# Kernel optimization log

Hardware: AMD Instinct MI355X
Metric: run time of the kernel (lower is better)

Reference implementation:

```python
import jax, jax.numpy as jnp
import numpy as np

N_NODES = 80000
N_EDGES = 1280000
D_NODE = 128
D_EDGE = 32
HID = 64
OUT = 32
EPS_GEN = 1e-7
EPS_BN = 1e-5


def _lin_init(key, fan_in, fan_out):
    return (jax.random.normal(key, (fan_in, fan_out), jnp.float32) / np.sqrt(fan_in))


def setup_inputs() -> dict:
    key = jax.random.key(0)
    ks = jax.random.split(key, 20)
    inp = {
        "x": jax.random.normal(ks[0], (N_NODES, D_NODE), jnp.float32),
        "edge_index": jax.random.randint(ks[1], (2, N_EDGES), 0, N_NODES, jnp.int32),
        "edge_attr": jax.random.normal(ks[2], (N_EDGES, D_EDGE), jnp.float32),
        # encoders
        "node_W": _lin_init(ks[3], D_NODE, HID), "node_b": jnp.zeros((HID,), jnp.float32),
        "edge_W": _lin_init(ks[4], D_EDGE, HID), "edge_b": jnp.zeros((HID,), jnp.float32),
        # GENConv layer 1 MLP: [HID -> 2HID (bias=False)] -> BN -> ReLU -> [2HID -> HID (bias=False)]
        "c1_W1": _lin_init(ks[5], HID, 2 * HID), "c1_g": jnp.ones((2 * HID,), jnp.float32), "c1_be": jnp.zeros((2 * HID,), jnp.float32), "c1_W2": _lin_init(ks[6], 2 * HID, HID),
        # GENConv layer 2
        "c2_W1": _lin_init(ks[7], HID, 2 * HID), "c2_g": jnp.ones((2 * HID,), jnp.float32), "c2_be": jnp.zeros((2 * HID,), jnp.float32), "c2_W2": _lin_init(ks[8], 2 * HID, HID),
        # edge update linears on concat(3*HID)
        "l1_W": _lin_init(ks[9], 3 * HID, HID), "l1_b": jnp.zeros((HID,), jnp.float32),
        "l2_W": _lin_init(ks[10], 3 * HID, OUT), "l2_b": jnp.zeros((OUT,), jnp.float32),
    }
    return inp


def _scatter_softmax_agg(msg, dst, n_nodes):
    # SoftmaxAggregation with t=1: per-destination, per-feature softmax weights
    m = jax.ops.segment_max(msg, dst, num_segments=n_nodes)  # [N, H]
    m = jnp.where(jnp.isfinite(m), m, 0.0)                   # nodes w/o in-edges
    ex = jnp.exp(msg - m[dst])                               # [E, H]
    denom = jax.ops.segment_sum(ex, dst, num_segments=n_nodes)
    alpha = ex / (denom[dst] + 1e-16)
    return jax.ops.segment_sum(msg * alpha, dst, num_segments=n_nodes)


def _batchnorm(h, gamma, beta):
    mu = jnp.mean(h, axis=0)
    var = jnp.var(h, axis=0)
    return (h - mu) * jax.lax.rsqrt(var + EPS_BN) * gamma + beta


def _genconv(x, src, dst, edge_attr, W1, g, be, W2):
    msg = jax.nn.relu(x[src] + edge_attr) + EPS_GEN          # [E, HID]
    agg = _scatter_softmax_agg(msg, dst, x.shape[0])         # [N, HID]
    h = agg + x
    h = jax.nn.relu(_batchnorm(h @ W1, g, be))
    return h @ W2


def reference(x, edge_index, edge_attr, node_W, node_b, edge_W, edge_b,
              c1_W1, c1_g, c1_be, c1_W2, c2_W1, c2_g, c2_be, c2_W2,
              l1_W, l1_b, l2_W, l2_b):
    src, dst = edge_index[0], edge_index[1]
    ea = edge_attr @ edge_W + edge_b                          # [E, HID]
    h = x @ node_W + node_b                                   # [N, HID]

    convs = [(c1_W1, c1_g, c1_be, c1_W2), (c2_W1, c2_g, c2_be, c2_W2)]
    lins = [(l1_W, l1_b), (l2_W, l2_b)]
    for (W1, g, be, W2), (lW, lb) in zip(convs, lins):
        h = jax.nn.relu(_genconv(h, src, dst, ea, W1, g, be, W2))
        # dropout is identity in eval mode
        ef = jnp.concatenate([h[src], ea, h[dst]], axis=-1)   # [E, 3*HID]
        ea = ef @ lW + lb
    return h, ea
```

## Files before the change

### kernel.cpp

```cpp
#include <hip/hip_runtime.h>
#include <hip/hip_bf16.h>

#define N_NODES 80000
#define N_EDGES 1280000
constexpr int DN = 128;
constexpr int DE = 32;
constexpr int H  = 64;
constexpr int H2 = 128;
constexpr float EPS_GEN = 1e-7f;
constexpr float EPS_BN  = 1e-5f;

typedef _Float16 f16x8 __attribute__((ext_vector_type(8)));
typedef _Float16 f16x4 __attribute__((ext_vector_type(4)));
typedef float f32x4 __attribute__((ext_vector_type(4)));

__device__ __forceinline__ void atomAddF(float* p, float v) {
  __hip_atomic_fetch_add(p, v, __ATOMIC_RELAXED, __HIP_MEMORY_SCOPE_AGENT);
}

struct PrepDesc { const float* W; _Float16* img; int K; int OC; int blkStart; };
struct PrepAll { PrepDesc d[8]; };

__global__ void k_prep_all(PrepAll P) {
  int b = blockIdx.x;
  int i = 0;
#pragma unroll
  for (int t = 1; t < 8; ++t)
    if (P.d[t].blkStart <= b) i = t;
  const PrepDesc D = P.d[i];
  int idx = (b - D.blkStart) * 256 + threadIdx.x;
  if (idx >= D.K * D.OC) return;
  int nslabK = D.K >> 5;
  int j = idx & 7, m16 = (idx >> 3) & 15, kg = (idx >> 7) & 3;
  int slab = idx >> 9;
  int kk = slab % nslabK, n2 = slab / nslabK;
  int k = kk * 32 + kg * 8 + j, n = n2 * 16 + m16;
  D.img[idx] = (_Float16)D.W[k * D.OC + n];
}

template <int K, int OC, bool IN16, bool AFFINE, bool BIAS,
          bool RELU_OUT, bool OUT16, bool OUT32, bool SCATOUT, bool STATS>
__global__ __launch_bounds__(256) void k_dense(
    const void* __restrict__ Ain, const _Float16* __restrict__ wimg,
    const float* __restrict__ bias, const float* __restrict__ sums,
    const float* __restrict__ g, const float* __restrict__ be,
    const int* __restrict__ posmap,
    _Float16* __restrict__ out16, float* __restrict__ out32,
    float* __restrict__ sums_out) {
  constexpr int NK = K / 32, NF = OC / 16;
  __shared__ float sSC[AFFINE ? H2 : 1], sSH[AFFINE ? H2 : 1];
  __shared__ float sStat[STATS ? 1024 : 1];
  const int tid = threadIdx.x, wv = tid >> 6, lane = tid & 63;
  const int m16 = lane & 15, kg = lane >> 4;
  const int rowbase = blockIdx.x * 64 + wv * 16;
  if constexpr (AFFINE) {
    for (int i = tid; i < H2; i += 256) {
      float mu  = sums[i] * (1.0f / N_NODES);
      float var = sums[H2 + i] * (1.0f / N_NODES) - mu * mu;
      float sc  = rsqrtf(var + EPS_BN) * g[i];
      sSC[i] = sc;
      sSH[i] = be[i] - mu * sc;
    }
    __syncthreads();
  }
  const int arow = rowbase + m16;
  f32x4 acc[NF];
#pragma unroll
  for (int n2 = 0; n2 < NF; ++n2) {
    float bv = BIAS ? bias[n2 * 16 + m16] : 0.0f;
    acc[n2] = (f32x4){bv, bv, bv, bv};
  }
  const _Float16* wp = wimg + (size_t)lane * 8;
#pragma unroll
  for (int kk = 0; kk < NK; ++kk) {
    f16x8 a;
    if constexpr (IN16) {
      const _Float16* ap = (const _Float16*)Ain + (size_t)arow * K + kg * 8 + kk * 32;
      a = *(const f16x8*)ap;
      if constexpr (AFFINE) {
#pragma unroll
        for (int j = 0; j < 8; ++j) {
          int f = kg * 8 + kk * 32 + j;
          float v = fmaxf(fmaf((float)a[j], sSC[f], sSH[f]), 0.0f);
          a[j] = (_Float16)v;
        }
      }
    } else {
      const float* ap = (const float*)Ain + (size_t)arow * K + kg * 8 + kk * 32;
      float4 v0 = *(const float4*)ap;
      float4 v1 = *(const float4*)(ap + 4);
      a = (f16x8){(_Float16)v0.x, (_Float16)v0.y, (_Float16)v0.z, (_Float16)v0.w,
                  (_Float16)v1.x, (_Float16)v1.y, (_Float16)v1.z, (_Float16)v1.w};
    }
#pragma unroll
    for (int n2 = 0; n2 < NF; ++n2) {
      f16x8 bb = *(const f16x8*)(wp + ((size_t)(n2 * NK + kk) << 9));
      acc[n2] = __builtin_amdgcn_mfma_f32_16x16x32_f16(a, bb, acc[n2], 0, 0, 0);
    }
  }
#pragma unroll
  for (int n2 = 0; n2 < NF; ++n2)
#pragma unroll
    for (int r = 0; r < 4; ++r) {
      float o = acc[n2][r];
      if constexpr (RELU_OUT) o = fmaxf(o, 0.0f);
      int orow = rowbase + kg * 4 + r;
      if constexpr (SCATOUT) orow = posmap[orow];
      size_t oi = (size_t)orow * OC + n2 * 16 + m16;
      if constexpr (OUT16) out16[oi] = (_Float16)o;
      if constexpr (OUT32) out32[oi] = o;
    }
  if constexpr (STATS) {
    static_assert(!STATS || NF == 8, "STATS assumes OC==128");
#pragma unroll
    for (int n2 = 0; n2 < NF; ++n2) {
      float s = acc[n2][0] + acc[n2][1] + acc[n2][2] + acc[n2][3];
      float q = acc[n2][0] * acc[n2][0] + acc[n2][1] * acc[n2][1] +
                acc[n2][2] * acc[n2][2] + acc[n2][3] * acc[n2][3];
      s += __shfl_xor(s, 16); s += __shfl_xor(s, 32);
      q += __shfl_xor(q, 16); q += __shfl_xor(q, 32);
      if (kg == 0) {
        sStat[wv * 128 + n2 * 16 + m16] = s;
        sStat[512 + wv * 128 + n2 * 16 + m16] = q;
      }
    }
    __syncthreads();
    {
      int which = tid >> 7, f = tid & 127;
      const float* b0 = sStat + which * 512;
      float v = b0[f] + b0[128 + f] + b0[256 + f] + b0[384 + f];
      atomAddF(&sums_out[which * H2 + f], v);
    }
  }
}

template <int OC, typename OUT_T, int T, bool SCAT>
__global__ __launch_bounds__(256) void k_edge_upd_srt(
    const _Float16* __restrict__ h, const _Float16* __restrict__ ea,
    const int4* __restrict__ eidsQ,
    const _Float16* __restrict__ wimg, const float* __restrict__ lb,
    OUT_T* __restrict__ eout) {
  constexpr int NF = OC / 16;
  __shared__ _Float16 sWf[NF * 6 * 512];
  __shared__ int sS[T * 64], sD[T * 64];
  __shared__ int sE[SCAT ? T * 64 : 1];
  const int tid = threadIdx.x, wv = tid >> 6, lane = tid & 63;
  const int m16 = lane & 15, kg = lane >> 4;
  const int p0 = blockIdx.x * (T * 64);

  for (int i = tid; i < T * 64; i += 256) {
    int4 t = eidsQ[p0 + i];
    sS[i] = t.y;
    sD[i] = t.z;
    if constexpr (SCAT) sE[i] = t.x;
  }
  {
    const float4* s4 = (const float4*)wimg;
    float4* d4 = (float4*)sWf;
    constexpr int NV = NF * 6 * 512 / 8;
    for (int i = tid; i < NV; i += 256) d4[i] = s4[i];
  }
  __syncthreads();
  const _Float16* wp = sWf + (size_t)lane * 8;

  float bias_[NF];
#pragma unroll
  for (int n2 = 0; n2 < NF; ++n2) bias_[n2] = lb[n2 * 16 + m16];

  f16x8 FA[6], FB[6];
  auto LOADA = [&](f16x8* F, int l) {
    const _Float16* a0 = h + (size_t)sS[l] * H + kg * 8;
    const _Float16* a1 = ea + (size_t)(p0 + l) * H + kg * 8;
    const _Float16* a2 = h + (size_t)sD[l] * H + kg * 8;
    F[0] = *(const f16x8*)a0;
    F[1] = *(const f16x8*)(a0 + 32);
    F[2] = *(const f16x8*)a1;
    F[3] = *(const f16x8*)(a1 + 32);
    F[4] = *(const f16x8*)a2;
    F[5] = *(const f16x8*)(a2 + 32);
  };
  auto COMPUTE = [&](const f16x8* F, int l) {
    f32x4 acc[NF];
#pragma unroll
    for (int n2 = 0; n2 < NF; ++n2)
      acc[n2] = (f32x4){bias_[n2], bias_[n2], bias_[n2], bias_[n2]};
#pragma unroll
    for (int kk = 0; kk < 6; ++kk)
#pragma unroll
      for (int n2 = 0; n2 < NF; ++n2) {
        f16x8 bb = *(const f16x8*)(wp + ((n2 * 6 + kk) << 9));
        acc[n2] = __builtin_amdgcn_mfma_f32_16x16x32_f16(F[kk], bb, acc[n2], 0, 0, 0);
      }
    const int lbase = l - m16;
#pragma unroll
    for (int n2 = 0; n2 < NF; ++n2)
#pragma unroll
      for (int r = 0; r < 4; ++r) {
        int lr = lbase + kg * 4 + r;
        int col = n2 * 16 + m16;
        if constexpr (SCAT)
          eout[(size_t)sE[lr] * OC + col] = (OUT_T)acc[n2][r];
        else
          eout[(size_t)(p0 + lr) * OC + col] = (OUT_T)acc[n2][r];
      }
  };

  const int l0 = wv * 16 + m16;
  LOADA(FA, l0);
  if (T > 1) LOADA(FB, l0 + 64);
#pragma unroll
  for (int t = 0; t < T; ++t) {
    if (t & 1) {
      COMPUTE(FB, l0 + t * 64);
      if (t + 2 < T) LOADA(FB, l0 + (t + 2) * 64);
    } else {
      COMPUTE(FA, l0 + t * 64);
      if (t + 2 < T) LOADA(FA, l0 + (t + 2) * 64);
    }
  }
}

__global__ void k_hist(const int* __restrict__ dst, int* cnt) {
  int e = blockIdx.x * blockDim.x + threadIdx.x;
  if (e < N_EDGES) atomicAdd(&cnt[dst[e]], 1);
}

__global__ void k_scan_blk(const int* __restrict__ cnt, int* __restrict__ bsum) {
  __shared__ int sh[256];
  int i = blockIdx.x * 256 + threadIdx.x;
  sh[threadIdx.x] = (i < N_NODES) ? cnt[i] : 0;
  __syncthreads();
  for (int s = 128; s > 0; s >>= 1) {
    if (threadIdx.x < s) sh[threadIdx.x] += sh[threadIdx.x + s];
    __syncthreads();
  }
  if (threadIdx.x == 0) bsum[blockIdx.x] = sh[0];
}

__global__ void k_scan_top(int* bsum, int nb) {
  __shared__ int sh[512];
  int t = threadIdx.x;
  int orig = (t < nb) ? bsum[t] : 0;
  sh[t] = orig;
  __syncthreads();
  for (int off = 1; off < 512; off <<= 1) {
    int v = (t >= off) ? sh[t - off] : 0;
    __syncthreads();
    sh[t] += v;
    __syncthreads();
  }
  if (t < nb) bsum[t] = sh[t] - orig;
}

__global__ void k_scan_fin(const int* __restrict__ cnt, const int* __restrict__ bsum,
                           int* __restrict__ start, int* __restrict__ cursor) {
  __shared__ int sh[256];
  int i = blockIdx.x * 256 + threadIdx.x;
  int t = threadIdx.x;
  int orig = (i < N_NODES) ? cnt[i] : 0;
  sh[t] = orig;
  __syncthreads();
  for (int off = 1; off < 256; off <<= 1) {
    int v = (t >= off) ? sh[t - off] : 0;
    __syncthreads();
    sh[t] += v;
    __syncthreads();
  }
  if (i < N_NODES) {
    int st = bsum[blockIdx.x] + sh[t] - orig;
    start[i] = st;
    cursor[i] = st;
  }
}

__global__ void k_scatter(const int* __restrict__ src, const int* __restrict__ dst,
                          int* cursor, int4* __restrict__ eidsQ, int* __restrict__ posOf) {
  int e = blockIdx.x * blockDim.x + threadIdx.x;
  if (e < N_EDGES) {
    int d = dst[e];
    int s = src[e];
    int pos = atomicAdd(&cursor[d], 1);
    eidsQ[pos] = make_int4(e, s, d, 0);
    posOf[e] = pos;
  }
}

__global__ __launch_bounds__(256) void k_agg_csr(
    const _Float16* __restrict__ h, const _Float16* __restrict__ ea_s,
    const int4* __restrict__ eidsQ, const int* __restrict__ start,
    const int* __restrict__ cnt, _Float16* __restrict__ hsum,
    float* __restrict__ sums_clr) {
  if (blockIdx.x == 0) sums_clr[threadIdx.x] = 0.0f;
  const int lane = threadIdx.x & 63;
  const int wid  = (int)((blockIdx.x * blockDim.x + threadIdx.x) >> 6);
  if (wid >= N_NODES) return;
  const int ep = lane >> 3, fg = lane & 7;
  const int s0 = start[wid], c = cnt[wid];
  float num[8] = {0.f, 0.f, 0.f, 0.f, 0.f, 0.f, 0.f, 0.f};
  float den[8] = {0.f, 0.f, 0.f, 0.f, 0.f, 0.f, 0.f, 0.f};
  if (c > 0) {
    const int nit = (c + 7) >> 3;
    int idx = min(ep, c - 1);
    int2 pe = *(const int2*)(eidsQ + s0 + idx);
    f16x8 hA = *(const f16x8*)(h + (size_t)pe.y * H + fg * 8);
    f16x8 eA = *(const f16x8*)(ea_s + (size_t)(s0 + idx) * H + fg * 8);
    bool vA = (ep < c);
    f16x8 hB = hA, eB = eA;
    bool vB = false;
    if (nit > 1) {
      idx = min(8 + ep, c - 1);
      pe = *(const int2*)(eidsQ + s0 + idx);
      hB = *(const f16x8*)(h + (size_t)pe.y * H + fg * 8);
      eB = *(const f16x8*)(ea_s + (size_t)(s0 + idx) * H + fg * 8);
      vB = (8 + ep < c);
    }
    for (int i = 0; i < nit; ++i) {
      f16x8 hc = hA, ec = eA;
      bool vc = vA;
      hA = hB; eA = eB; vA = vB;
      if (i + 2 < nit) {
        idx = min((i + 2) * 8 + ep, c - 1);
        pe = *(const int2*)(eidsQ + s0 + idx);
        hB = *(const f16x8*)(h + (size_t)pe.y * H + fg * 8);
        eB = *(const f16x8*)(ea_s + (size_t)(s0 + idx) * H + fg * 8);
        vB = ((i + 2) * 8 + ep < c);
      }
#pragma unroll
      for (int j = 0; j < 8; ++j) {
        float m = fmaxf((float)hc[j] + (float)ec[j], 0.0f) + EPS_GEN;
        float ex = vc ? __expf(m) : 0.0f;
        num[j] = fmaf(m, ex, num[j]);
        den[j] += ex;
      }
    }
  }
#pragma unroll
  for (int j = 0; j < 8; ++j) {
    num[j] += __shfl_xor(num[j], 8);
    num[j] += __shfl_xor(num[j], 16);
    num[j] += __shfl_xor(num[j], 32);
    den[j] += __shfl_xor(den[j], 8);
    den[j] += __shfl_xor(den[j], 16);
    den[j] += __shfl_xor(den[j], 32);
  }
  if (ep == 0) {
    f16x8 hs = *(const f16x8*)(h + (size_t)wid * H + fg * 8);
    f16x8 o;
#pragma unroll
    for (int j = 0; j < 8; ++j)
      o[j] = (_Float16)(num[j] / (den[j] + 1e-16f) + (float)hs[j]);
    *(f16x8*)(hsum + (size_t)wid * H + fg * 8) = o;
  }
}

extern "C" void kernel_launch(void* const* d_in, const int* in_sizes, int n_in,
                              void* d_out, int out_size, void* d_ws, size_t ws_size,
                              hipStream_t stream) {
  (void)in_sizes; (void)n_in; (void)out_size; (void)ws_size;
  const float* x      = (const float*)d_in[0];
  const int*   eidx   = (const int*)d_in[1];
  const float* eattr  = (const float*)d_in[2];
  const float* node_W = (const float*)d_in[3];
  const float* node_b = (const float*)d_in[4];
  const float* edge_W = (const float*)d_in[5];
  const float* edge_b = (const float*)d_in[6];
  const float* c1_W1  = (const float*)d_in[7];
  const float* c1_g   = (const float*)d_in[8];
  const float* c1_be  = (const float*)d_in[9];
  const float* c1_W2  = (const float*)d_in[10];
  const float* c2_W1  = (const float*)d_in[11];
  const float* c2_g   = (const float*)d_in[12];
  const float* c2_be  = (const float*)d_in[13];
  const float* c2_W2  = (const float*)d_in[14];
  const float* l1_W   = (const float*)d_in[15];
  const float* l1_b   = (const float*)d_in[16];
  const float* l2_W   = (const float*)d_in[17];
  const float* l2_b   = (const float*)d_in[18];

  const int* src = eidx;
  const int* dst = eidx + N_EDGES;

  char* wsb = (char*)d_ws;
  size_t off = 0;
  _Float16* ea_s  = (_Float16*)(wsb + off); off += (size_t)N_EDGES * H * 2;
  _Float16* hA16  = (_Float16*)(wsb + off); off += (size_t)N_NODES * H * 2;
  _Float16* hB16  = (_Float16*)(wsb + off); off += (size_t)N_NODES * H * 2;
  _Float16* hC16  = (_Float16*)(wsb + off); off += (size_t)N_NODES * H * 2;
  _Float16* hsum16= (_Float16*)(wsb + off); off += (size_t)N_NODES * H * 2;
  _Float16* h3    = (_Float16*)(wsb + off); off += (size_t)N_NODES * H2 * 2;
  float* sums     = (float*)(wsb + off);    off += 256 * 4;
  int* cnt        = (int*)(wsb + off);      off += (size_t)N_NODES * 4;
  int* startA     = (int*)(wsb + off);      off += (size_t)N_NODES * 4;
  int* cursor     = (int*)(wsb + off);      off += (size_t)N_NODES * 4;
  int* bsum       = (int*)(wsb + off);      off += 512 * 4;
  int4* eidsQ     = (int4*)(wsb + off);     off += (size_t)N_EDGES * 16;
  int* posOf      = (int*)(wsb + off);      off += (size_t)N_EDGES * 4;
  _Float16* wE    = (_Float16*)(wsb + off); off += DE * H * 2;
  _Float16* wN    = (_Float16*)(wsb + off); off += DN * H * 2;
  _Float16* w1a   = (_Float16*)(wsb + off); off += H * H2 * 2;
  _Float16* w1b   = (_Float16*)(wsb + off); off += H * H2 * 2;
  _Float16* w2a   = (_Float16*)(wsb + off); off += H2 * H * 2;
  _Float16* w2b   = (_Float16*)(wsb + off); off += H2 * H * 2;
  _Float16* wL1   = (_Float16*)(wsb + off); off += 3 * H * H * 2;
  _Float16* wL2   = (_Float16*)(wsb + off); off += 3 * H * 32 * 2;

  float* h_out  = (float*)d_out;
  float* ea_out = (float*)d_out + (size_t)N_NODES * H;

  constexpr int NB = (N_NODES + 255) / 256;

  PrepAll P;
  P.d[0] = {edge_W, wE, DE, H, 0};
  P.d[1] = {node_W, wN, DN, H, 8};
  P.d[2] = {c1_W1, w1a, H, H2, 40};
  P.d[3] = {c2_W1, w1b, H, H2, 72};
  P.d[4] = {c1_W2, w2a, H2, H, 104};
  P.d[5] = {c2_W2, w2b, H2, H, 136};
  P.d[6] = {l1_W, wL1, 192, H, 168};
  P.d[7] = {l2_W, wL2, 192, 32, 216};
  k_prep_all<<<240, 256, 0, stream>>>(P);

  hipMemsetAsync(cnt, 0, N_NODES * 4, stream);
  k_hist<<<(N_EDGES + 255) / 256, 256, 0, stream>>>(dst, cnt);
  k_scan_blk<<<NB, 256, 0, stream>>>(cnt, bsum);
  k_scan_top<<<1, 512, 0, stream>>>(bsum, NB);
  k_scan_fin<<<NB, 256, 0, stream>>>(cnt, bsum, startA, cursor);
  k_scatter<<<(N_EDGES + 255) / 256, 256, 0, stream>>>(src, dst, cursor, eidsQ, posOf);

  k_dense<DE, H, false, false, true, false, true, false, true, false>
      <<<N_EDGES / 64, 256, 0, stream>>>(eattr, wE, edge_b, nullptr, nullptr, nullptr,
                                         posOf, ea_s, nullptr, nullptr);
  k_dense<DN, H, false, false, true, false, true, false, false, false>
      <<<N_NODES / 64, 256, 0, stream>>>(x, wN, node_b, nullptr, nullptr, nullptr,
                                         nullptr, hA16, nullptr, nullptr);

  k_agg_csr<<<(N_NODES + 3) / 4, 256, 0, stream>>>(hA16, ea_s, eidsQ, startA, cnt, hsum16, sums);
  k_dense<H, H2, true, false, false, false, true, false, false, true>
      <<<N_NODES / 64, 256, 0, stream>>>(hsum16, w1a, nullptr, nullptr, nullptr, nullptr,
                                         nullptr, h3, nullptr, sums);
  k_dense<H2, H, true, true, false, true, true, false, false, false>
      <<<N_NODES / 64, 256, 0, stream>>>(h3, w2a, nullptr, sums, c1_g, c1_be,
                                         nullptr, hB16, nullptr, nullptr);
  k_edge_upd_srt<64, _Float16, 8, false>
      <<<N_EDGES / 512, 256, 0, stream>>>(hB16, ea_s, eidsQ, wL1, l1_b, ea_s);

  k_agg_csr<<<(N_NODES + 3) / 4, 256, 0, stream>>>(hB16, ea_s, eidsQ, startA, cnt, hsum16, sums);
  k_dense<H, H2, true, false, false, false, true, false, false, true>
      <<<N_NODES / 64, 256, 0, stream>>>(hsum16, w1b, nullptr, nullptr, nullptr, nullptr,
                                         nullptr, h3, nullptr, sums);
  k_dense<H2, H, true, true, false, true, true, true, false, false>
      <<<N_NODES / 64, 256, 0, stream>>>(h3, w2b, nullptr, sums, c2_g, c2_be,
                                         nullptr, hC16, h_out, nullptr);
  k_edge_upd_srt<32, float, 8, true>
      <<<N_EDGES / 512, 256, 0, stream>>>(hC16, ea_s, eidsQ, wL2, l2_b, ea_out);
}
```

Before: 663.9 us.

## Record per-edge rank in histogram with padded counters; drop scatter atomics

Measured after the change: 602.3 us. 1.1x faster.

```diff
diff --git a/kernel.cpp b/kernel.cpp
--- a/kernel.cpp
+++ b/kernel.cpp
@@ -7,6 +7,7 @@
 constexpr int DE = 32;
 constexpr int H  = 64;
 constexpr int H2 = 128;
+constexpr int CSTRIDE = 32;
 constexpr float EPS_GEN = 1e-7f;
 constexpr float EPS_BN  = 1e-5f;
 
@@ -220,15 +221,16 @@
   }
 }
 
-__global__ void k_hist(const int* __restrict__ dst, int* cnt) {
+__global__ void k_rank(const int* __restrict__ dst, int* cntPad, int* __restrict__ rank) {
   int e = blockIdx.x * blockDim.x + threadIdx.x;
-  if (e < N_EDGES) atomicAdd(&cnt[dst[e]], 1);
-}
-
-__global__ void k_scan_blk(const int* __restrict__ cnt, int* __restrict__ bsum) {
+  if (e < N_EDGES)
+    rank[e] = atomicAdd(&cntPad[(size_t)dst[e] * CSTRIDE], 1);
+}
+
+__global__ void k_scan_blk(const int* __restrict__ cntPad, int* __restrict__ bsum) {
   __shared__ int sh[256];
   int i = blockIdx.x * 256 + threadIdx.x;
-  sh[threadIdx.x] = (i < N_NODES) ? cnt[i] : 0;
+  sh[threadIdx.x] = (i < N_NODES) ? cntPad[(size_t)i * CSTRIDE] : 0;
   __syncthreads();
   for (int s = 128; s > 0; s >>= 1) {
     if (threadIdx.x < s) sh[threadIdx.x] += sh[threadIdx.x + s];
@@ -252,12 +254,12 @@
   if (t < nb) bsum[t] = sh[t] - orig;
 }
 
-__global__ void k_scan_fin(const int* __restrict__ cnt, const int* __restrict__ bsum,
-                           int* __restrict__ start, int* __restrict__ cursor) {
+__global__ void k_scan_fin(const int* __restrict__ cntPad, const int* __restrict__ bsum,
+                           int* __restrict__ start, int* __restrict__ cntC) {
   __shared__ int sh[256];
   int i = blockIdx.x * 256 + threadIdx.x;
   int t = threadIdx.x;
-  int orig = (i < N_NODES) ? cnt[i] : 0;
+  int orig = (i < N_NODES) ? cntPad[(size_t)i * CSTRIDE] : 0;
   sh[t] = orig;
   __syncthreads();
   for (int off = 1; off < 256; off <<= 1) {
@@ -267,20 +269,19 @@
     __syncthreads();
   }
   if (i < N_NODES) {
-    int st = bsum[blockIdx.x] + sh[t] - orig;
-    start[i] = st;
-    cursor[i] = st;
+    start[i] = bsum[blockIdx.x] + sh[t] - orig;
+    cntC[i] = orig;
   }
 }
 
 __global__ void k_scatter(const int* __restrict__ src, const int* __restrict__ dst,
-                          int* cursor, int4* __restrict__ eidsQ, int* __restrict__ posOf) {
+                          const int* __restrict__ rank, const int* __restrict__ start,
+                          int4* __restrict__ eidsQ, int* __restrict__ posOf) {
   int e = blockIdx.x * blockDim.x + threadIdx.x;
   if (e < N_EDGES) {
     int d = dst[e];
-    int s = src[e];
-    int pos = atomicAdd(&cursor[d], 1);
-    eidsQ[pos] = make_int4(e, s, d, 0);
+    int pos = start[d] + rank[e];
+    eidsQ[pos] = make_int4(e, src[e], d, 0);
     posOf[e] = pos;
   }
 }
@@ -389,10 +390,11 @@
   _Float16* hsum16= (_Float16*)(wsb + off); off += (size_t)N_NODES * H * 2;
   _Float16* h3    = (_Float16*)(wsb + off); off += (size_t)N_NODES * H2 * 2;
   float* sums     = (float*)(wsb + off);    off += 256 * 4;
-  int* cnt        = (int*)(wsb + off);      off += (size_t)N_NODES * 4;
+  int* cntPad     = (int*)(wsb + off);      off += (size_t)N_NODES * CSTRIDE * 4;
   int* startA     = (int*)(wsb + off);      off += (size_t)N_NODES * 4;
-  int* cursor     = (int*)(wsb + off);      off += (size_t)N_NODES * 4;
+  int* cntC       = (int*)(wsb + off);      off += (size_t)N_NODES * 4;
   int* bsum       = (int*)(wsb + off);      off += 512 * 4;
+  int* rankE      = (int*)(wsb + off);      off += (size_t)N_EDGES * 4;
   int4* eidsQ     = (int4*)(wsb + off);     off += (size_t)N_EDGES * 16;
   int* posOf      = (int*)(wsb + off);      off += (size_t)N_EDGES * 4;
   _Float16* wE    = (_Float16*)(wsb + off); off += DE * H * 2;
@@ -420,12 +422,12 @@
   P.d[7] = {l2_W, wL2, 192, 32, 216};
   k_prep_all<<<240, 256, 0, stream>>>(P);
 
-  hipMemsetAsync(cnt, 0, N_NODES * 4, stream);
-  k_hist<<<(N_EDGES + 255) / 256, 256, 0, stream>>>(dst, cnt);
-  k_scan_blk<<<NB, 256, 0, stream>>>(cnt, bsum);
+  hipMemsetAsync(cntPad, 0, (size_t)N_NODES * CSTRIDE * 4, stream);
+  k_rank<<<(N_EDGES + 255) / 256, 256, 0, stream>>>(dst, cntPad, rankE);
+  k_scan_blk<<<NB, 256, 0, stream>>>(cntPad, bsum);
   k_scan_top<<<1, 512, 0, stream>>>(bsum, NB);
-  k_scan_fin<<<NB, 256, 0, stream>>>(cnt, bsum, startA, cursor);
-  k_scatter<<<(N_EDGES + 255) / 256, 256, 0, stream>>>(src, dst, cursor, eidsQ, posOf);
+  k_scan_fin<<<NB, 256, 0, stream>>>(cntPad, bsum, startA, cntC);
+  k_scatter<<<(N_EDGES + 255) / 256, 256, 0, stream>>>(src, dst, rankE, startA, eidsQ, posOf);
 
   k_dense<DE, H, false, false, true, false, true, false, true, false>
       <<<N_EDGES / 64, 256, 0, stream>>>(eattr, wE, edge_b, nullptr, nullptr, nullptr,
@@ -434,23 +436,23 @@
       <<<N_NODES / 64, 256, 0, stream>>>(x, wN, node_b, nullptr, nullptr, nullptr,
                                          nullptr, hA16, nullptr, nullptr);
 
-  k_agg_csr<<<(N_NODES + 3) / 4, 256, 0, stream>>>(hA16, ea_s, eidsQ, startA, cnt, hsum16, sums);
+  k_agg_csr<<<(N_NODES + 3) / 4, 256, 0, stream>>>(hA16, ea_s, eidsQ, startA, cntC, hsum16, sums);
   k_dense<H, H2, true, false, false, false, true, false, false, true>
       <<<N_NODES / 64, 256, 0, stream>>>(hsum16, w1a, nullptr, nullptr, nullptr, nullptr,
                                          nullptr, h3, nullptr, sums);
   k_dense<H2, H, true, true, false, true, true, false, false, false>
       <<<N_NODES / 64, 256, 0, stream>>>(h3, w2a, nullptr, sums, c1_g, c1_be,
                                          nullptr, hB16, nullptr, nullptr);
-  k_edge_upd_srt<64, _Float16, 8, false>
-      <<<N_EDGES / 512, 256, 0, stream>>>(hB16, ea_s, eidsQ, wL1, l1_b, ea_s);
-
-  k_agg_csr<<<(N_NODES + 3) / 4, 256, 0, stream>>>(hB16, ea_s, eidsQ, startA, cnt, hsum16, sums);
+  k_edge_upd_srt<64, _Float16, 16, false>
+      <<<N_EDGES / 1024, 256, 0, stream>>>(hB16, ea_s, eidsQ, wL1, l1_b, ea_s);
+
+  k_agg_csr<<<(N_NODES + 3) / 4, 256, 0, stream>>>(hB16, ea_s, eidsQ, startA, cntC, hsum16, sums);
   k_dense<H, H2, true, false, false, false, true, false, false, true>
       <<<N_NODES / 64, 256, 0, stream>>>(hsum16, w1b, nullptr, nullptr, nullptr, nullptr,
                                          nullptr, h3, nullptr, sums);
   k_dense<H2, H, true, true, false, true, true, true, false, false>
       <<<N_NODES / 64, 256, 0, stream>>>(h3, w2b, nullptr, sums, c2_g, c2_be,
                                          nullptr, hC16, h_out, nullptr);
-  k_edge_upd_srt<32, float, 8, true>
-      <<<N_EDGES / 512, 256, 0, stream>>>(hC16, ea_s, eidsQ, wL2, l2_b, ea_out);
-}
+  k_edge_upd_srt<32, float, 16, true>
+      <<<N_EDGES / 1024, 256, 0, stream>>>(hC16, ea_s, eidsQ, wL2, l2_b, ea_out);
+}
```
